# Performance work log

Measured on AMD Instinct MI355X. Metric: run time of the kernel, lower is better.

The kernel has to match this reference:

```python
import jax, jax.numpy as jnp
import numpy as np

B, G, H, K = 2, 16, 128, 8      # batch, grid side, hidden, edges per grid point
TG = B * G ** 3                  # total grid points = 8192
E = TG * K                       # total edges = 65536
N = 2048                         # total atoms
EPS = 1e-5


def _bn(x, g, b):
    # eval-mode BatchNorm3d with running_mean=0, running_var=1
    s = g / jnp.sqrt(1.0 + EPS)
    return x * s[None, :, None, None, None] + b[None, :, None, None, None]


def _conv(x, w, pad):
    return jax.lax.conv_general_dilated(
        x, w, window_strides=(1, 1, 1), padding=[(pad, pad)] * 3,
        dimension_numbers=("NCDHW", "OIDHW", "NCDHW"))


def _mlp2(x, w1, b1, w2, b2, act):
    return act(x @ w1 + b1) @ w2 + b2


def setup_inputs() -> dict:
    key = jax.random.key(0)
    ks = jax.random.split(key, 16)
    def nrm(k, shape, scale=1.0):
        return jax.random.normal(k, shape, dtype=jnp.float32) * scale
    def lin(k, i, o):
        return nrm(k, (i, o), 1.0 / np.sqrt(i))
    return {
        "node_embedding": nrm(ks[0], (N, H)),
        "node_pos": nrm(ks[1], (N, 3)),
        "grid_pos": nrm(ks[2], (TG, 3)),
        "edge_row": jax.random.randint(ks[3], (E,), 0, N),
        # every grid point covered K times -> bincount never zero (matches original's div-by-bincount)
        "edge_col": jnp.repeat(jnp.arange(TG), K),
        "edge_w1": lin(ks[4], 6, H),    "edge_b1": jnp.zeros(H),
        "edge_w2": lin(ks[5], H, H),    "edge_b2": jnp.zeros(H),
        "msg_w1": lin(ks[6], 2 * H, H), "msg_b1": jnp.zeros(H),
        "msg_w2": lin(ks[7], H, H),     "msg_b2": jnp.zeros(H),
        "upd_w1": lin(ks[8], H, H),     "upd_b1": jnp.zeros(H),
        "upd_w2": lin(ks[9], H, H),     "upd_b2": jnp.zeros(H),
        "in_gamma": jnp.ones(H), "in_beta": jnp.zeros(H),
        "blk_conv1": nrm(ks[10], (3, H, H, 3, 3, 3), 1.0 / np.sqrt(H * 27)),
        "blk_bn1_g": jnp.ones((3, H)), "blk_bn1_b": jnp.zeros((3, H)),
        "blk_conv2": nrm(ks[11], (3, H, H, 3, 3, 3), 1.0 / np.sqrt(H * 27)),
        "blk_bn2_g": jnp.ones((3, H)), "blk_bn2_b": jnp.zeros((3, H)),
        "blk_conv5": nrm(ks[12], (3, H, H, 5, 5, 5), 1.0 / np.sqrt(H * 125)),
        "blk_bns_g": jnp.ones((3, H)), "blk_bns_b": jnp.zeros((3, H)),
        "fc_w": lin(ks[13], H, 20), "fc_b": jnp.zeros(20),
    }


def reference(node_embedding, node_pos, grid_pos, edge_row, edge_col,
              edge_w1, edge_b1, edge_w2, edge_b2,
              msg_w1, msg_b1, msg_w2, msg_b2,
              upd_w1, upd_b1, upd_w2, upd_b2,
              in_gamma, in_beta,
              blk_conv1, blk_bn1_g, blk_bn1_b,
              blk_conv2, blk_bn2_g, blk_bn2_b,
              blk_conv5, blk_bns_g, blk_bns_b,
              fc_w, fc_b):
    silu = jax.nn.silu
    # ---- MPNN message: gather -> edge MLP -> message MLP ----
    edge_attr = jnp.concatenate([node_pos[edge_row], grid_pos[edge_col]], axis=-1)  # [E,6]
    pos_emb = _mlp2(edge_attr, edge_w1, edge_b1, edge_w2, edge_b2, silu)            # [E,H]
    msg_in = jnp.concatenate([node_embedding[edge_row], pos_emb], axis=-1)          # [E,2H]
    message = _mlp2(msg_in, msg_w1, msg_b1, msg_w2, msg_b2, silu)                   # [E,H]
    # ---- scatter-mean onto grid points (global_add_pool / bincount) ----
    agg = jax.ops.segment_sum(message, edge_col, num_segments=TG)
    cnt = jax.ops.segment_sum(jnp.ones((E,), jnp.float32), edge_col, num_segments=TG)
    agg = agg / cnt[:, None]
    x = _mlp2(agg, upd_w1, upd_b1, upd_w2, upd_b2, silu)                            # [TG,H]
    # ---- to dense grid, channels-first ----
    x = x.reshape(B, G, G, G, H).transpose(0, 4, 1, 2, 3)                           # [B,H,G,G,G]
    x = _bn(x, in_gamma, in_beta)
    # ---- 3 residual blocks (eval BN, dropout identity) ----
    for i in range(3):
        left = jax.nn.relu(_bn(_conv(x, blk_conv1[i], 1), blk_bn1_g[i], blk_bn1_b[i]))
        left = _bn(_conv(left, blk_conv2[i], 1), blk_bn2_g[i], blk_bn2_b[i])
        short = _bn(_conv(x, blk_conv5[i], 2), blk_bns_g[i], blk_bns_b[i])
        x = jax.nn.relu(left + short)
    # ---- global max pool (kernel == spatial size) + fc + log_softmax ----
    pooled = x.max(axis=(2, 3, 4))                                                  # [B,H]
    logits = pooled @ fc_w + fc_b                                                   # [B,20]
    return jax.nn.log_softmax(logits, axis=-1)
```

## Files before the change

kernel.cpp:

```cpp
#include <hip/hip_runtime.h>
#include <math.h>


#define EPS_BN 1e-5f

typedef _Float16 f16x8 __attribute__((ext_vector_type(8)));
typedef float f32x4 __attribute__((ext_vector_type(4)));

struct us4 { unsigned short x, y, z, w; };

__device__ __forceinline__ float silu_f(float x) {
  return x / (1.0f + __expf(-x));
}
__device__ __forceinline__ unsigned short f2h(float x) {
  union { _Float16 h; unsigned short u; } v; v.h = (_Float16)x; return v.u;
}
__device__ __forceinline__ float h2f(unsigned short u) {
  union { unsigned short u; _Float16 h; } v; v.u = u; return (float)v.h;
}

template<int AMODE, int KTOT>
__global__ __launch_bounds__(256, 2)
void gemm_k(const float* __restrict__ A,
            const float* __restrict__ W,
            const float* __restrict__ bias,
            const float* __restrict__ pscale,
            const float* __restrict__ pshift,
            float* __restrict__ C,
            int act, int obf)
{
  __shared__ __align__(16) float As[32][68];
  __shared__ __align__(16) float Bs[32][128];
  const int t = threadIdx.x;
  const int mbase = blockIdx.x * 64;
  const int m0 = (t >> 4) << 2;
  const int nA = (t & 15) << 2;
  const int ml = t >> 2;
  const int ks = (t & 3) << 3;

  float acc[4][8];
#pragma unroll
  for (int i = 0; i < 4; i++)
#pragma unroll
    for (int j = 0; j < 8; j++) acc[i][j] = 0.f;

  for (int k0 = 0; k0 < KTOT; k0 += 32) {
    {
      const float* src = A + (size_t)(mbase + ml) * KTOT + (k0 + ks);
      const float4 a0 = *(const float4*)src;
      const float4 a1 = *(const float4*)(src + 4);
      As[ks+0][ml]=a0.x; As[ks+1][ml]=a0.y; As[ks+2][ml]=a0.z; As[ks+3][ml]=a0.w;
      As[ks+4][ml]=a1.x; As[ks+5][ml]=a1.y; As[ks+6][ml]=a1.z; As[ks+7][ml]=a1.w;
    }
    {
      const int kl = t >> 3;
      const int ns = (t & 7) << 4;
      const float* wsrc = W + (size_t)(k0 + kl) * 128 + ns;
      *(float4*)&Bs[kl][ns +  0] = *(const float4*)(wsrc + 0);
      *(float4*)&Bs[kl][ns +  4] = *(const float4*)(wsrc + 4);
      *(float4*)&Bs[kl][ns +  8] = *(const float4*)(wsrc + 8);
      *(float4*)&Bs[kl][ns + 12] = *(const float4*)(wsrc + 12);
    }
    __syncthreads();
#pragma unroll 8
    for (int kk = 0; kk < 32; kk++) {
      const float4 av = *(const float4*)&As[kk][m0];
      const float4 b0 = *(const float4*)&Bs[kk][nA];
      const float4 b1 = *(const float4*)&Bs[kk][nA + 64];
      const float a[4]  = {av.x, av.y, av.z, av.w};
      const float bb[8] = {b0.x, b0.y, b0.z, b0.w, b1.x, b1.y, b1.z, b1.w};
#pragma unroll
      for (int i = 0; i < 4; i++)
#pragma unroll
        for (int j = 0; j < 8; j++)
          acc[i][j] = fmaf(a[i], bb[j], acc[i][j]);
    }
    __syncthreads();
  }

  const float rs = rsqrtf(1.f + EPS_BN);
#pragma unroll
  for (int i = 0; i < 4; i++) {
    const size_t row = (size_t)(mbase + m0 + i);
    float v[8];
#pragma unroll
    for (int j = 0; j < 8; j++) {
      const int col = (j < 4) ? (nA + j) : (nA + 60 + j);
      float x = acc[i][j] + bias[col];
      if (act == 1) x = silu_f(x);
      if (pscale) x = fmaf(x, pscale[col] * rs, pshift[col]);
      v[j] = x;
    }
    if (obf) {
      unsigned short* Cb = (unsigned short*)C;
      us4 r0, r1;
      r0.x=f2h(v[0]); r0.y=f2h(v[1]); r0.z=f2h(v[2]); r0.w=f2h(v[3]);
      r1.x=f2h(v[4]); r1.y=f2h(v[5]); r1.z=f2h(v[6]); r1.w=f2h(v[7]);
      *(us4*)&Cb[row * 128 + nA]      = r0;
      *(us4*)&Cb[row * 128 + nA + 64] = r1;
    } else {
      *(float4*)&C[row * 128 + nA]      = make_float4(v[0], v[1], v[2], v[3]);
      *(float4*)&C[row * 128 + nA + 64] = make_float4(v[4], v[5], v[6], v[7]);
    }
  }
}

__global__ __launch_bounds__(256)
void wpack_g_k(const float* __restrict__ w, unsigned short* __restrict__ wp,
               int total)
{
  const int i = blockIdx.x * 256 + threadIdx.x;
  if (i >= total) return;
  const int j   = i & 7;
  const int l   = (i >> 3) & 63;
  const int nt  = (i >> 9) & 7;
  const int kq  = (i >> 12) & 3;
  const int tap = i >> 14;
  const int k = tap * 128 + kq * 32 + (l >> 4) * 8 + j;
  const int n = nt * 16 + (l & 15);
  wp[i] = f2h(w[(size_t)k * 128 + n]);
}

__global__ __launch_bounds__(256)
void cvt_k(const float* __restrict__ src, unsigned short* __restrict__ dst, int n)
{
  const int i = blockIdx.x * 256 + threadIdx.x;
  if (i < n) dst[i] = f2h(src[i]);
}

__device__ __forceinline__ void stage_b(const unsigned short* g,
                                        unsigned short* dl) {
#pragma unroll
  for (int r = 0; r < 8; r++)
    __builtin_amdgcn_global_load_lds(
        (const __attribute__((address_space(1))) unsigned int*)(g + r * 2048),
        (__attribute__((address_space(3))) unsigned int*)(dl + r * 2048),
        16, 0, 0);
}

__device__ __forceinline__ void mfma_tile(const unsigned short* Aswz,
                                          const unsigned short* Bb,
                                          int mb, int nb, int lx, int lq, int l,
                                          f32x4 acc[2][4]) {
  const int xm = lx & 7;
#pragma unroll
  for (int kq = 0; kq < 4; kq++) {
    f16x8 a0 = *(const f16x8*)(Aswz + (size_t)(((mb + 0) * 16 + lx) * 16 + ((kq * 4 + lq) ^ xm)) * 8);
    f16x8 a1 = *(const f16x8*)(Aswz + (size_t)(((mb + 1) * 16 + lx) * 16 + ((kq * 4 + lq) ^ xm)) * 8);
    const unsigned short* bbase = Bb + (size_t)((kq * 8 + nb) * 64 + l) * 8;
#pragma unroll
    for (int j = 0; j < 4; j++) {
      f16x8 bv = *(const f16x8*)(bbase + (size_t)j * 512);
      acc[0][j] = __builtin_amdgcn_mfma_f32_16x16x32_f16(a0, bv, acc[0][j], 0, 0, 0);
      acc[1][j] = __builtin_amdgcn_mfma_f32_16x16x32_f16(a1, bv, acc[1][j], 0, 0, 0);
    }
  }
}

__device__ __forceinline__ void epi_h(const f32x4 acc[2][4],
                                      const float* bias, int act,
                                      unsigned short* dst,
                                      int mb, int nb, int lx, int lq) {
#pragma unroll
  for (int i = 0; i < 2; i++)
#pragma unroll
    for (int r = 0; r < 4; r++) {
      const int rowloc = (mb + i) * 16 + lq * 4 + r;
#pragma unroll
      for (int j = 0; j < 4; j++) {
        const int col = (nb + j) * 16 + lx;
        float x = acc[i][j][r] + bias[col];
        if (act) x = silu_f(x);
        dst[rowloc * 128 + col] = f2h(x);
      }
    }
}

__device__ __forceinline__ void restage(const unsigned short* src,
                                        unsigned short* Aswz,
                                        int rowl, int seg) {
#pragma unroll
  for (int uu = 0; uu < 4; uu++) {
    uint4 v = *(const uint4*)(src + rowl * 128 + seg * 32 + uu * 8);
    const int u = seg * 4 + uu;
    *(uint4*)(Aswz + (size_t)(rowl * 16 + (u ^ (rowl & 7))) * 8) = v;
  }
}

__global__ __launch_bounds__(256, 1)
void mpnn_k(const unsigned short* __restrict__ emb16,
            const int* __restrict__ rows,
            const int* __restrict__ cols,
            const float* __restrict__ npos,
            const float* __restrict__ gpos,
            const float* __restrict__ ew1,
            const float* __restrict__ eb1,
            const float* __restrict__ eb2,
            const float* __restrict__ mb1,
            const float* __restrict__ mb2,
            const unsigned short* __restrict__ wall,
            float* __restrict__ aggout)
{
  __shared__ __align__(16) unsigned short Aswz[8192];
  __shared__ __align__(16) unsigned short Cpl[8192];
  __shared__ __align__(16) unsigned short Bb[16384];

  const int t = threadIdx.x;
  const int mbase = blockIdx.x * 64;
  const int l = t & 63, w = t >> 6;
  const int lx = l & 15, lq = l >> 4;
  const int mb = (w >> 1) << 1;
  const int nb = (w & 1) << 2;
  const int rowl = t >> 2;
  const int seg  = t & 3;

  const int e = mbase + rowl;
  const int rr = rows[e];
  const int gg = cols[e];
  const float at0 = npos[rr*3+0], at1 = npos[rr*3+1], at2 = npos[rr*3+2];
  const float at3 = gpos[gg*3+0], at4 = gpos[gg*3+1], at5 = gpos[gg*3+2];

#pragma unroll
  for (int uu = 0; uu < 4; uu++) {
    union { unsigned short h[8]; uint4 v; } pk;
#pragma unroll
    for (int jj = 0; jj < 8; jj++) {
      const int k = seg * 32 + uu * 8 + jj;
      float s = eb1[k];
      s = fmaf(at0, ew1[      k], s);
      s = fmaf(at1, ew1[128 + k], s);
      s = fmaf(at2, ew1[256 + k], s);
      s = fmaf(at3, ew1[384 + k], s);
      s = fmaf(at4, ew1[512 + k], s);
      s = fmaf(at5, ew1[640 + k], s);
      pk.h[jj] = f2h(silu_f(s));
    }
    const int u = seg * 4 + uu;
    *(uint4*)(Aswz + (size_t)(rowl * 16 + (u ^ (rowl & 7))) * 8) = pk.v;
  }
  stage_b(wall + t * 8, Bb + t * 8);
  __syncthreads();

  f32x4 acc1[2][4];
#pragma unroll
  for (int i = 0; i < 2; i++)
#pragma unroll
    for (int j = 0; j < 4; j++) acc1[i][j] = (f32x4){0.f,0.f,0.f,0.f};
  mfma_tile(Aswz, Bb, mb, nb, lx, lq, l, acc1);
  __syncthreads();

  epi_h(acc1, eb2, 0, Cpl, mb, nb, lx, lq);
  {
    const unsigned short* src = emb16 + (size_t)rr * 128 + seg * 32;
#pragma unroll
    for (int uu = 0; uu < 4; uu++) {
      const uint4 v = *(const uint4*)(src + uu * 8);
      const int u = seg * 4 + uu;
      *(uint4*)(Aswz + (size_t)(rowl * 16 + (u ^ (rowl & 7))) * 8) = v;
    }
  }
  stage_b(wall + 16384 + t * 8, Bb + t * 8);
  __syncthreads();

  f32x4 acc2[2][4];
#pragma unroll
  for (int i = 0; i < 2; i++)
#pragma unroll
    for (int j = 0; j < 4; j++) acc2[i][j] = (f32x4){0.f,0.f,0.f,0.f};
  mfma_tile(Aswz, Bb, mb, nb, lx, lq, l, acc2);
  __syncthreads();

  stage_b(wall + 32768 + t * 8, Bb + t * 8);
  restage(Cpl, Aswz, rowl, seg);
  __syncthreads();

  mfma_tile(Aswz, Bb, mb, nb, lx, lq, l, acc2);
  __syncthreads();

  epi_h(acc2, mb1, 1, Cpl, mb, nb, lx, lq);
  stage_b(wall + 49152 + t * 8, Bb + t * 8);
  __syncthreads();

  restage(Cpl, Aswz, rowl, seg);
  __syncthreads();

  f32x4 acc3[2][4];
#pragma unroll
  for (int i = 0; i < 2; i++)
#pragma unroll
    for (int j = 0; j < 4; j++) acc3[i][j] = (f32x4){0.f,0.f,0.f,0.f};
  mfma_tile(Aswz, Bb, mb, nb, lx, lq, l, acc3);
  __syncthreads();

  float* Bf = (float*)Bb;
#pragma unroll
  for (int i = 0; i < 2; i++)
#pragma unroll
    for (int r = 0; r < 4; r++) {
      const int rowloc = (mb + i) * 16 + lq * 4 + r;
#pragma unroll
      for (int j = 0; j < 4; j++) {
        const int col = (nb + j) * 16 + lx;
        Bf[rowloc * 128 + col] = acc3[i][j][r] + mb2[col];
      }
    }
  __syncthreads();

#pragma unroll
  for (int qq = 0; qq < 4; qq++) {
    const int q = t * 4 + qq;
    const int g = q >> 7, c = q & 127;
    float s = 0.f;
#pragma unroll
    for (int r = 0; r < 8; r++) s += Bf[(g * 8 + r) * 128 + c];
    aggout[(size_t)((mbase >> 3) + g) * 128 + c] = s * 0.125f;
  }
}

__global__ __launch_bounds__(256)
void wpack_k(const float* __restrict__ w, unsigned short* __restrict__ wp,
             int T, int total)
{
  const int i = blockIdx.x * 256 + threadIdx.x;
  if (i >= total) return;
  const int j  = i & 7;
  const int l  = (i >> 3) & 63;
  const int nt = (i >> 9) & 7;
  const int kq = (i >> 12) & 3;
  const int r  = i >> 14;
  const int tap = r % T;
  const int ib  = r / T;
  const int o = nt * 16 + (l & 15);
  const int c = kq * 32 + (l >> 4) * 8 + j;
  wp[i] = f2h(w[((size_t)(ib * 128 + o) * 128 + c) * T + tap]);
}

template<int KS>
__global__ __launch_bounds__(256, 1)
void convmf_k(const unsigned short* __restrict__ xin,
              const unsigned short* __restrict__ wpack,
              float* __restrict__ part)
{
  constexpr int P  = KS / 2;
  constexpr int SW = 16 + 2 * P;
  __shared__ __align__(16) unsigned short Ab[4 * SW * 128];
  __shared__ __align__(16) unsigned short Bb[16384];

  const int t   = threadIdx.x;
  const int bx  = blockIdx.x;
  const int kd  = bx >> 7;
  const int rem = bx & 127;
  const int b   = rem >> 6;
  const int z   = (rem >> 2) & 15;
  const int y0  = (rem & 3) << 2;
  const int zz  = z + kd - P;
  float* pout = part + (size_t)kd * (8192 * 128);
  const size_t obase = ((size_t)((b * 16 + z) * 16 + y0) * 16) * 128;

  if ((unsigned)zz >= 16u) {
    float4 zf = make_float4(0, 0, 0, 0);
    float4* dst = (float4*)(pout + obase);
    for (int i = t; i < 2048; i += 256) dst[i] = zf;
    return;
  }

  const int l  = t & 63, w = t >> 6;
  const int lx = l & 15, lq = l >> 4;
  const int mb = (w >> 1) << 1;
  const int nb = (w & 1) << 2;

  f32x4 acc[2][4];
#pragma unroll
  for (int i = 0; i < 2; i++)
#pragma unroll
    for (int j = 0; j < 4; j++) acc[i][j] = (f32x4){0.f, 0.f, 0.f, 0.f};

  const unsigned short* inplane = xin + ((size_t)(b * 16 + zz) * 256) * 128;
  const unsigned short* wkd = wpack + (size_t)(kd * KS * KS) * 16384;

  for (int kh = 0; kh < KS; kh++) {
    __syncthreads();
    for (int idx = t; idx < 4 * SW * 16; idx += 256) {
      const int ry = idx / (SW * 16);
      const int r2 = idx - ry * (SW * 16);
      const int xs = r2 >> 4;
      const int u  = r2 & 15;
      const int y  = y0 + ry + kh - P;
      const int x  = xs - P;
      uint4 val = make_uint4(0, 0, 0, 0);
      if ((unsigned)y < 16u && (unsigned)x < 16u)
        val = *(const uint4*)(inplane + ((size_t)(y * 16 + x)) * 128 + u * 8);
      const int du = (ry * SW + xs) * 16 + (u ^ (xs & 7));
      *(uint4*)(Ab + (size_t)du * 8) = val;
    }
    const unsigned short* wkh = wkd + (size_t)(kh * KS) * 16384;
    for (int kw = 0; kw < KS; kw++) {
      __syncthreads();
      stage_b(wkh + (size_t)kw * 16384 + t * 8, Bb + t * 8);
      __syncthreads();
      const int xsw = lx + kw;
      const int xm  = xsw & 7;
#pragma unroll
      for (int kq = 0; kq < 4; kq++) {
        f16x8 a0 = *(const f16x8*)(Ab + (size_t)(((mb + 0) * SW + xsw) * 16 + ((kq * 4 + lq) ^ xm)) * 8);
        f16x8 a1 = *(const f16x8*)(Ab + (size_t)(((mb + 1) * SW + xsw) * 16 + ((kq * 4 + lq) ^ xm)) * 8);
        const unsigned short* bbase = Bb + (size_t)((kq * 8 + nb) * 64 + l) * 8;
#pragma unroll
        for (int j = 0; j < 4; j++) {
          f16x8 bv = *(const f16x8*)(bbase + (size_t)j * 512);
          acc[0][j] = __builtin_amdgcn_mfma_f32_16x16x32_f16(a0, bv, acc[0][j], 0, 0, 0);
          acc[1][j] = __builtin_amdgcn_mfma_f32_16x16x32_f16(a1, bv, acc[1][j], 0, 0, 0);
        }
      }
    }
  }

#pragma unroll
  for (int i = 0; i < 2; i++) {
    const int my = mb + i;
#pragma unroll
    for (int r = 0; r < 4; r++) {
      const size_t vrow = obase + (size_t)(my * 16 + lq * 4 + r) * 128;
#pragma unroll
      for (int j = 0; j < 4; j++)
        pout[vrow + (nb + j) * 16 + lx] = acc[i][j][r];
    }
  }
}

__global__ __launch_bounds__(256)
void combine1_k(const float* __restrict__ p,
                const float* __restrict__ g, const float* __restrict__ be,
                unsigned short* __restrict__ o)
{
  const int i = blockIdx.x * 256 + threadIdx.x;
  const size_t off = (size_t)i * 4;
  const int c = (i & 31) * 4;
  float4 a0 = *(const float4*)(p + off);
  float4 a1 = *(const float4*)(p + 1048576 + off);
  float4 a2 = *(const float4*)(p + 2097152 + off);
  const float rs = rsqrtf(1.f + EPS_BN);
  float4 gg = *(const float4*)(g + c);
  float4 bb = *(const float4*)(be + c);
  float v0 = fmaxf(fmaf(a0.x + a1.x + a2.x, gg.x * rs, bb.x), 0.f);
  float v1 = fmaxf(fmaf(a0.y + a1.y + a2.y, gg.y * rs, bb.y), 0.f);
  float v2 = fmaxf(fmaf(a0.z + a1.z + a2.z, gg.z * rs, bb.z), 0.f);
  float v3 = fmaxf(fmaf(a0.w + a1.w + a2.w, gg.w * rs, bb.w), 0.f);
  us4 r; r.x = f2h(v0); r.y = f2h(v1); r.z = f2h(v2); r.w = f2h(v3);
  *(us4*)(o + off) = r;
}

__global__ __launch_bounds__(256)
void combine2_k(const float* __restrict__ p2, const float* __restrict__ p5,
                const float* __restrict__ g2, const float* __restrict__ b2,
                const float* __restrict__ gs, const float* __restrict__ bs,
                unsigned short* __restrict__ o)
{
  const int i = blockIdx.x * 256 + threadIdx.x;
  const size_t off = (size_t)i * 4;
  const int c = (i & 31) * 4;
  float4 s2 = *(const float4*)(p2 + off);
  {
    float4 a1 = *(const float4*)(p2 + 1048576 + off);
    float4 a2 = *(const float4*)(p2 + 2097152 + off);
    s2.x += a1.x + a2.x; s2.y += a1.y + a2.y;
    s2.z += a1.z + a2.z; s2.w += a1.w + a2.w;
  }
  float4 s5 = *(const float4*)(p5 + off);
#pragma unroll
  for (int gi = 1; gi < 5; gi++) {
    float4 a = *(const float4*)(p5 + (size_t)gi * 1048576 + off);
    s5.x += a.x; s5.y += a.y; s5.z += a.z; s5.w += a.w;
  }
  const float rs = rsqrtf(1.f + EPS_BN);
  float4 gg2 = *(const float4*)(g2 + c);
  float4 bb2 = *(const float4*)(b2 + c);
  float4 ggs = *(const float4*)(gs + c);
  float4 bbs = *(const float4*)(bs + c);
  float v0 = fmaxf(fmaf(s2.x, gg2.x * rs, bb2.x) + fmaf(s5.x, ggs.x * rs, bbs.x), 0.f);
  float v1 = fmaxf(fmaf(s2.y, gg2.y * rs, bb2.y) + fmaf(s5.y, ggs.y * rs, bbs.y), 0.f);
  float v2 = fmaxf(fmaf(s2.z, gg2.z * rs, bb2.z) + fmaf(s5.z, ggs.z * rs, bbs.z), 0.f);
  float v3 = fmaxf(fmaf(s2.w, gg2.w * rs, bb2.w) + fmaf(s5.w, ggs.w * rs, bbs.w), 0.f);
  us4 r; r.x = f2h(v0); r.y = f2h(v1); r.z = f2h(v2); r.w = f2h(v3);
  *(us4*)(o + off) = r;
}

__global__ __launch_bounds__(256)
void pool_partial_k(const unsigned short* __restrict__ xg, float* __restrict__ pmax)
{
  __shared__ float red[256];
  const int bz = blockIdx.x;
  const int t = threadIdx.x;
  const int c = t & 127;
  const int h = t >> 7;
  const unsigned short* base = xg + (size_t)bz * 256 * 128;
  float m = -3.4e38f;
  for (int i = 0; i < 128; i++)
    m = fmaxf(m, h2f(base[(size_t)(h * 128 + i) * 128 + c]));
  red[t] = m;
  __syncthreads();
  if (t < 128) pmax[bz * 128 + t] = fmaxf(red[t], red[t + 128]);
}

__global__ __launch_bounds__(256)
void final_k(const float* __restrict__ pmax,
             const float* __restrict__ fc_w,
             const float* __restrict__ fc_b,
             float* __restrict__ outp)
{
  __shared__ float pool[2][128];
  __shared__ float lg[2][20];
  const int t = threadIdx.x;
  const int b = t >> 7;
  const int c = t & 127;
  float m = -3.4e38f;
  for (int zi = 0; zi < 16; zi++)
    m = fmaxf(m, pmax[(b * 16 + zi) * 128 + c]);
  pool[b][c] = m;
  __syncthreads();
  if (t < 40) {
    const int bb = t / 20, j = t % 20;
    float l = fc_b[j];
    for (int cc = 0; cc < 128; cc++)
      l = fmaf(pool[bb][cc], fc_w[cc * 20 + j], l);
    lg[bb][j] = l;
  }
  __syncthreads();
  if (t < 2) {
    float mx = -3.4e38f;
    for (int j = 0; j < 20; j++) mx = fmaxf(mx, lg[t][j]);
    float s = 0.f;
    for (int j = 0; j < 20; j++) s += expf(lg[t][j] - mx);
    const float ls = mx + logf(s);
    for (int j = 0; j < 20; j++) outp[t * 20 + j] = lg[t][j] - ls;
  }
}

extern "C" void kernel_launch(void* const* d_in, const int* in_sizes, int n_in,
                              void* d_out, int out_size, void* d_ws, size_t ws_size,
                              hipStream_t stream) {
  (void)in_sizes; (void)n_in; (void)out_size; (void)ws_size;
  const float* node_embedding = (const float*)d_in[0];
  const float* node_pos  = (const float*)d_in[1];
  const float* grid_pos  = (const float*)d_in[2];
  const int*   edge_row  = (const int*)d_in[3];
  const int*   edge_col  = (const int*)d_in[4];
  const float* edge_w1   = (const float*)d_in[5];
  const float* edge_b1   = (const float*)d_in[6];
  const float* edge_w2   = (const float*)d_in[7];
  const float* edge_b2   = (const float*)d_in[8];
  const float* msg_w1    = (const float*)d_in[9];
  const float* msg_b1    = (const float*)d_in[10];
  const float* msg_w2    = (const float*)d_in[11];
  const float* msg_b2    = (const float*)d_in[12];
  const float* upd_w1    = (const float*)d_in[13];
  const float* upd_b1    = (const float*)d_in[14];
  const float* upd_w2    = (const float*)d_in[15];
  const float* upd_b2    = (const float*)d_in[16];
  const float* in_gamma  = (const float*)d_in[17];
  const float* in_beta   = (const float*)d_in[18];
  const float* blk_conv1 = (const float*)d_in[19];
  const float* blk_bn1_g = (const float*)d_in[20];
  const float* blk_bn1_b = (const float*)d_in[21];
  const float* blk_conv2 = (const float*)d_in[22];
  const float* blk_bn2_g = (const float*)d_in[23];
  const float* blk_bn2_b = (const float*)d_in[24];
  const float* blk_conv5 = (const float*)d_in[25];
  const float* blk_bns_g = (const float*)d_in[26];
  const float* blk_bns_b = (const float*)d_in[27];
  const float* fc_w      = (const float*)d_in[28];
  const float* fc_b      = (const float*)d_in[29];

  float* ws = (float*)d_ws;
  unsigned short* wp31 = (unsigned short*)ws;
  unsigned short* wp32 = (unsigned short*)(ws + 663552);
  unsigned short* wp5  = (unsigned short*)(ws + 1327104);
  float* p1   = ws + 4400128;
  float* p2   = ws + 7545856;
  float* p5   = ws + 10691584;
  unsigned short* xg0 = (unsigned short*)(ws + 16000000);
  unsigned short* xg1 = (unsigned short*)(ws + 16524288);
  unsigned short* tg  = (unsigned short*)(ws + 17048576);
  float* agg  = ws + 17572864;
  float* u1   = ws + 18621440;
  float* pmax = ws + 19670016;
  unsigned short* emb16  = (unsigned short*)(ws + 19675136);
  unsigned short* wg_all = (unsigned short*)(ws + 19806208);
  float* outF = (float*)d_out;

  cvt_k<<<1024, 256, 0, stream>>>(node_embedding, emb16, 2048 * 128);
  wpack_g_k<<<64, 256, 0, stream>>>(edge_w2, wg_all, 16384);
  wpack_g_k<<<128, 256, 0, stream>>>(msg_w1, wg_all + 16384, 32768);
  wpack_g_k<<<64, 256, 0, stream>>>(msg_w2, wg_all + 49152, 16384);
  wpack_k<<<5184, 256, 0, stream>>>(blk_conv1, wp31, 27, 3 * 27 * 16384);
  wpack_k<<<5184, 256, 0, stream>>>(blk_conv2, wp32, 27, 3 * 27 * 16384);
  wpack_k<<<24000, 256, 0, stream>>>(blk_conv5, wp5, 125, 3 * 125 * 16384);

  mpnn_k<<<1024, 256, 0, stream>>>(
      emb16, edge_row, edge_col, node_pos, grid_pos, edge_w1, edge_b1,
      edge_b2, msg_b1, msg_b2, wg_all, agg);

  gemm_k<0, 128><<<128, 256, 0, stream>>>(
      agg, upd_w1, upd_b1, nullptr, nullptr, u1, 1, 0);
  gemm_k<0, 128><<<128, 256, 0, stream>>>(
      u1, upd_w2, upd_b2, in_gamma, in_beta, (float*)xg0, 0, 1);

  const unsigned short* xin = xg0;
  unsigned short* xout = xg1;
  for (int i = 0; i < 3; i++) {
    convmf_k<3><<<384, 256, 0, stream>>>(xin, wp31 + (size_t)i * 27 * 16384, p1);
    combine1_k<<<1024, 256, 0, stream>>>(p1, blk_bn1_g + i * 128, blk_bn1_b + i * 128, tg);
    convmf_k<3><<<384, 256, 0, stream>>>(tg, wp32 + (size_t)i * 27 * 16384, p2);
    convmf_k<5><<<640, 256, 0, stream>>>(xin, wp5 + (size_t)i * 125 * 16384, p5);
    combine2_k<<<1024, 256, 0, stream>>>(p2, p5,
        blk_bn2_g + i * 128, blk_bn2_b + i * 128,
        blk_bns_g + i * 128, blk_bns_b + i * 128, xout);
    unsigned short* tmp = (unsigned short*)xin;
    xin = xout;
    xout = tmp;
  }

  pool_partial_k<<<32, 256, 0, stream>>>(xin, pmax);
  final_k<<<1, 256, 0, stream>>>(pmax, fc_w, fc_b, outF);
}
```

Measured before the change: 525.8 us.

## Double-buffer conv weight staging in half-K chunks to overlap loads with MFMA

The direct-conv MFMA kernel now splits each per-tap weight tile into two K-halves and keeps two LDS buffers. It issues the async global-to-LDS load for the next half-tile before computing on the current one, replacing the old load-barrier-compute sequence that left the matrix units idle while weights arrived. The cost is twice as many barriers per tap, and each barrier still waits for every outstanding load, so a prefetch only has one half-tile of compute to hide behind. The final iteration also issues one redundant load.

```diff
diff --git a/kernel.cpp b/kernel.cpp
--- a/kernel.cpp
+++ b/kernel.cpp
@@ -132,6 +132,16 @@
                                         unsigned short* dl) {
 #pragma unroll
   for (int r = 0; r < 8; r++)
+    __builtin_amdgcn_global_load_lds(
+        (const __attribute__((address_space(1))) unsigned int*)(g + r * 2048),
+        (__attribute__((address_space(3))) unsigned int*)(dl + r * 2048),
+        16, 0, 0);
+}
+
+__device__ __forceinline__ void stage_half(const unsigned short* g,
+                                           unsigned short* dl) {
+#pragma unroll
+  for (int r = 0; r < 4; r++)
     __builtin_amdgcn_global_load_lds(
         (const __attribute__((address_space(1))) unsigned int*)(g + r * 2048),
         (__attribute__((address_space(3))) unsigned int*)(dl + r * 2048),
@@ -343,8 +353,9 @@
 {
   constexpr int P  = KS / 2;
   constexpr int SW = 16 + 2 * P;
+  constexpr int NU = 2 * KS * KS;
   __shared__ __align__(16) unsigned short Ab[4 * SW * 128];
-  __shared__ __align__(16) unsigned short Bb[16384];
+  __shared__ __align__(16) unsigned short Bb[2][8192];
 
   const int t   = threadIdx.x;
   const int bx  = blockIdx.x;
@@ -378,39 +389,49 @@
   const unsigned short* inplane = xin + ((size_t)(b * 16 + zz) * 256) * 128;
   const unsigned short* wkd = wpack + (size_t)(kd * KS * KS) * 16384;
 
+  stage_half(wkd + t * 8, Bb[0] + t * 8);
+
+  int u = 0;
   for (int kh = 0; kh < KS; kh++) {
     __syncthreads();
     for (int idx = t; idx < 4 * SW * 16; idx += 256) {
       const int ry = idx / (SW * 16);
       const int r2 = idx - ry * (SW * 16);
       const int xs = r2 >> 4;
-      const int u  = r2 & 15;
+      const int uu = r2 & 15;
       const int y  = y0 + ry + kh - P;
       const int x  = xs - P;
       uint4 val = make_uint4(0, 0, 0, 0);
       if ((unsigned)y < 16u && (unsigned)x < 16u)
-        val = *(const uint4*)(inplane + ((size_t)(y * 16 + x)) * 128 + u * 8);
-      const int du = (ry * SW + xs) * 16 + (u ^ (xs & 7));
+        val = *(const uint4*)(inplane + ((size_t)(y * 16 + x)) * 128 + uu * 8);
+      const int du = (ry * SW + xs) * 16 + (uu ^ (xs & 7));
       *(uint4*)(Ab + (size_t)du * 8) = val;
     }
-    const unsigned short* wkh = wkd + (size_t)(kh * KS) * 16384;
     for (int kw = 0; kw < KS; kw++) {
-      __syncthreads();
-      stage_b(wkh + (size_t)kw * 16384 + t * 8, Bb + t * 8);
-      __syncthreads();
       const int xsw = lx + kw;
       const int xm  = xsw & 7;
 #pragma unroll
-      for (int kq = 0; kq < 4; kq++) {
-        f16x8 a0 = *(const f16x8*)(Ab + (size_t)(((mb + 0) * SW + xsw) * 16 + ((kq * 4 + lq) ^ xm)) * 8);
-        f16x8 a1 = *(const f16x8*)(Ab + (size_t)(((mb + 1) * SW + xsw) * 16 + ((kq * 4 + lq) ^ xm)) * 8);
-        const unsigned short* bbase = Bb + (size_t)((kq * 8 + nb) * 64 + l) * 8;
-#pragma unroll
-        for (int j = 0; j < 4; j++) {
-          f16x8 bv = *(const f16x8*)(bbase + (size_t)j * 512);
-          acc[0][j] = __builtin_amdgcn_mfma_f32_16x16x32_f16(a0, bv, acc[0][j], 0, 0, 0);
-          acc[1][j] = __builtin_amdgcn_mfma_f32_16x16x32_f16(a1, bv, acc[1][j], 0, 0, 0);
+      for (int h = 0; h < 2; h++) {
+        __syncthreads();
+        {
+          const int nu = (u + 1 < NU) ? (u + 1) : u;
+          stage_half(wkd + (size_t)nu * 8192 + t * 8, Bb[(u + 1) & 1] + t * 8);
         }
+        const unsigned short* Bcur = Bb[u & 1];
+#pragma unroll
+        for (int kqh = 0; kqh < 2; kqh++) {
+          const int kq = h * 2 + kqh;
+          f16x8 a0 = *(const f16x8*)(Ab + (size_t)(((mb + 0) * SW + xsw) * 16 + ((kq * 4 + lq) ^ xm)) * 8);
+          f16x8 a1 = *(const f16x8*)(Ab + (size_t)(((mb + 1) * SW + xsw) * 16 + ((kq * 4 + lq) ^ xm)) * 8);
+          const unsigned short* bbase = Bcur + (size_t)((kqh * 8 + nb) * 64 + l) * 8;
+#pragma unroll
+          for (int j = 0; j < 4; j++) {
+            f16x8 bv = *(const f16x8*)(bbase + (size_t)j * 512);
+            acc[0][j] = __builtin_amdgcn_mfma_f32_16x16x32_f16(a0, bv, acc[0][j], 0, 0, 0);
+            acc[1][j] = __builtin_amdgcn_mfma_f32_16x16x32_f16(a1, bv, acc[1][j], 0, 0, 0);
+          }
+        }
+        u++;
       }
     }
   }
```

Result: slower. 540.7 us (+2.8%).

## Halve conv block to two waves with larger per-wave register tiles

Applied to the files above, without the earlier changes.

The MFMA conv kernel now runs with 128 threads (2 waves) instead of 4. Each wave computes all 4 output rows over 64 channels, a 4x4 accumulator grid, so every B fragment loaded from LDS feeds four MFMAs instead of two. The weight-staging and input-staging loops are adapted to the smaller thread count. The trade-off is higher register pressure, and fewer waves per block to hide the staging latency and the barriers.

```diff
diff --git a/kernel.cpp b/kernel.cpp
--- a/kernel.cpp
+++ b/kernel.cpp
@@ -135,6 +135,16 @@
     __builtin_amdgcn_global_load_lds(
         (const __attribute__((address_space(1))) unsigned int*)(g + r * 2048),
         (__attribute__((address_space(3))) unsigned int*)(dl + r * 2048),
+        16, 0, 0);
+}
+
+__device__ __forceinline__ void stage_b_128t(const unsigned short* g,
+                                             unsigned short* dl) {
+#pragma unroll
+  for (int r = 0; r < 16; r++)
+    __builtin_amdgcn_global_load_lds(
+        (const __attribute__((address_space(1))) unsigned int*)(g + r * 1024),
+        (__attribute__((address_space(3))) unsigned int*)(dl + r * 1024),
         16, 0, 0);
 }
 
@@ -336,7 +346,7 @@
 }
 
 template<int KS>
-__global__ __launch_bounds__(256, 1)
+__global__ __launch_bounds__(128, 1)
 void convmf_k(const unsigned short* __restrict__ xin,
               const unsigned short* __restrict__ wpack,
               float* __restrict__ part)
@@ -360,18 +370,17 @@
   if ((unsigned)zz >= 16u) {
     float4 zf = make_float4(0, 0, 0, 0);
     float4* dst = (float4*)(pout + obase);
-    for (int i = t; i < 2048; i += 256) dst[i] = zf;
+    for (int i = t; i < 2048; i += 128) dst[i] = zf;
     return;
   }
 
   const int l  = t & 63, w = t >> 6;
   const int lx = l & 15, lq = l >> 4;
-  const int mb = (w >> 1) << 1;
-  const int nb = (w & 1) << 2;
-
-  f32x4 acc[2][4];
-#pragma unroll
-  for (int i = 0; i < 2; i++)
+  const int nb = w << 2;
+
+  f32x4 acc[4][4];
+#pragma unroll
+  for (int i = 0; i < 4; i++)
 #pragma unroll
     for (int j = 0; j < 4; j++) acc[i][j] = (f32x4){0.f, 0.f, 0.f, 0.f};
 
@@ -380,50 +389,52 @@
 
   for (int kh = 0; kh < KS; kh++) {
     __syncthreads();
-    for (int idx = t; idx < 4 * SW * 16; idx += 256) {
+    for (int idx = t; idx < 4 * SW * 16; idx += 128) {
       const int ry = idx / (SW * 16);
       const int r2 = idx - ry * (SW * 16);
       const int xs = r2 >> 4;
-      const int u  = r2 & 15;
+      const int uu = r2 & 15;
       const int y  = y0 + ry + kh - P;
       const int x  = xs - P;
       uint4 val = make_uint4(0, 0, 0, 0);
       if ((unsigned)y < 16u && (unsigned)x < 16u)
-        val = *(const uint4*)(inplane + ((size_t)(y * 16 + x)) * 128 + u * 8);
-      const int du = (ry * SW + xs) * 16 + (u ^ (xs & 7));
+        val = *(const uint4*)(inplane + ((size_t)(y * 16 + x)) * 128 + uu * 8);
+      const int du = (ry * SW + xs) * 16 + (uu ^ (xs & 7));
       *(uint4*)(Ab + (size_t)du * 8) = val;
     }
     const unsigned short* wkh = wkd + (size_t)(kh * KS) * 16384;
     for (int kw = 0; kw < KS; kw++) {
       __syncthreads();
-      stage_b(wkh + (size_t)kw * 16384 + t * 8, Bb + t * 8);
+      stage_b_128t(wkh + (size_t)kw * 16384 + t * 8, Bb + t * 8);
       __syncthreads();
       const int xsw = lx + kw;
       const int xm  = xsw & 7;
 #pragma unroll
       for (int kq = 0; kq < 4; kq++) {
-        f16x8 a0 = *(const f16x8*)(Ab + (size_t)(((mb + 0) * SW + xsw) * 16 + ((kq * 4 + lq) ^ xm)) * 8);
-        f16x8 a1 = *(const f16x8*)(Ab + (size_t)(((mb + 1) * SW + xsw) * 16 + ((kq * 4 + lq) ^ xm)) * 8);
+        f16x8 a[4];
+#pragma unroll
+        for (int m = 0; m < 4; m++)
+          a[m] = *(const f16x8*)(Ab + (size_t)((m * SW + xsw) * 16 + ((kq * 4 + lq) ^ xm)) * 8);
         const unsigned short* bbase = Bb + (size_t)((kq * 8 + nb) * 64 + l) * 8;
 #pragma unroll
         for (int j = 0; j < 4; j++) {
           f16x8 bv = *(const f16x8*)(bbase + (size_t)j * 512);
-          acc[0][j] = __builtin_amdgcn_mfma_f32_16x16x32_f16(a0, bv, acc[0][j], 0, 0, 0);
-          acc[1][j] = __builtin_amdgcn_mfma_f32_16x16x32_f16(a1, bv, acc[1][j], 0, 0, 0);
+#pragma unroll
+          for (int m = 0; m < 4; m++)
+            acc[m][j] = __builtin_amdgcn_mfma_f32_16x16x32_f16(a[m], bv, acc[m][j], 0, 0, 0);
         }
       }
     }
   }
 
 #pragma unroll
-  for (int i = 0; i < 2; i++) {
-    const int my = mb + i;
+  for (int m = 0; m < 4; m++) {
 #pragma unroll
     for (int r = 0; r < 4; r++) {
-      const size_t vrow = obase + (size_t)(my * 16 + lq * 4 + r) * 128;
+      const size_t vrow = obase + (size_t)(m * 16 + lq * 4 + r) * 128;
 #pragma unroll
       for (int j = 0; j < 4; j++)
-        pout[vrow + (nb + j) * 16 + lx] = acc[i][j][r];
+        pout[vrow + (nb + j) * 16 + lx] = acc[m][j][r];
     }
   }
 }
@@ -608,10 +619,10 @@
   const unsigned short* xin = xg0;
   unsigned short* xout = xg1;
   for (int i = 0; i < 3; i++) {
-    convmf_k<3><<<384, 256, 0, stream>>>(xin, wp31 + (size_t)i * 27 * 16384, p1);
+    convmf_k<3><<<384, 128, 0, stream>>>(xin, wp31 + (size_t)i * 27 * 16384, p1);
     combine1_k<<<1024, 256, 0, stream>>>(p1, blk_bn1_g + i * 128, blk_bn1_b + i * 128, tg);
-    convmf_k<3><<<384, 256, 0, stream>>>(tg, wp32 + (size_t)i * 27 * 16384, p2);
-    convmf_k<5><<<640, 256, 0, stream>>>(xin, wp5 + (size_t)i * 125 * 16384, p5);
+    convmf_k<3><<<384, 128, 0, stream>>>(tg, wp32 + (size_t)i * 27 * 16384, p2);
+    convmf_k<5><<<640, 128, 0, stream>>>(xin, wp5 + (size_t)i * 125 * 16384, p5);
     combine2_k<<<1024, 256, 0, stream>>>(p2, p5,
         blk_bn2_g + i * 128, blk_bn2_b + i * 128,
         blk_bns_g + i * 128, blk_bns_b + i * 128, xout);
```

Result: slower. 587.0 us (+11.6%).
